# Kernel tuning notes

Hardware: AMD Instinct MI355X
Metric: run time of the kernel (lower is better)

The kernel has to match this reference:

```python
import jax, jax.numpy as jnp
import numpy as np

D_MODEL = 1024
NUM_HEADS = 16
D_HEAD = D_MODEL // NUM_HEADS
LN_EPS = 1e-5


def setup_inputs() -> dict:
    key = jax.random.key(0)
    ks = jax.random.split(key, 10)
    s = 1.0 / np.sqrt(D_MODEL)
    inp = {
        "batch": jax.random.normal(ks[0], (4, 2048, D_MODEL), dtype=jnp.float32),
        "wq": jax.random.uniform(ks[1], (D_MODEL, D_MODEL), jnp.float32, -s, s),
        "bq": jax.random.uniform(ks[2], (D_MODEL,), jnp.float32, -s, s),
        "wk": jax.random.uniform(ks[3], (D_MODEL, D_MODEL), jnp.float32, -s, s),
        "bk": jax.random.uniform(ks[4], (D_MODEL,), jnp.float32, -s, s),
        "wv": jax.random.uniform(ks[5], (D_MODEL, D_MODEL), jnp.float32, -s, s),
        "bv": jax.random.uniform(ks[6], (D_MODEL,), jnp.float32, -s, s),
        "wo": jax.random.uniform(ks[7], (D_MODEL, D_MODEL), jnp.float32, -s, s),
        "bo": jax.random.uniform(ks[8], (D_MODEL,), jnp.float32, -s, s),
        "ln_g": jnp.ones((D_MODEL,), jnp.float32),
        "ln_b": jnp.zeros((D_MODEL,), jnp.float32),
    }
    return inp


def reference(batch, wq, bq, wk, bk, wv, bv, wo, bo, ln_g, ln_b):
    B, S, D = batch.shape
    # QKV projections (torch Linear: x @ W.T + b)
    q = (batch @ wq.T + bq).reshape(B, S, NUM_HEADS, D_HEAD)
    k = (batch @ wk.T + bk).reshape(B, S, NUM_HEADS, D_HEAD)
    v = (batch @ wv.T + bv).reshape(B, S, NUM_HEADS, D_HEAD)
    # attention scores [B, H, S, S]
    scores = jnp.einsum("bqhd,bkhd->bhqk", q, k) / np.sqrt(D_HEAD).astype(np.float32)
    # (original masked_fill is not in-place -> mask has no effect; omitted)
    probs = jax.nn.softmax(scores, axis=-1)
    attn = jnp.einsum("bhqk,bkhd->bqhd", probs, v).reshape(B, S, D)
    residual = attn @ wo.T + bo  # dropout = identity (eval mode)
    x = batch + residual
    mu = jnp.mean(x, axis=-1, keepdims=True)
    var = jnp.mean(jnp.square(x - mu), axis=-1, keepdims=True)
    return (x - mu) / jnp.sqrt(var + LN_EPS) * ln_g + ln_b
```

## Files before the change

### kernel.cpp

```cpp
#include <hip/hip_runtime.h>

typedef __bf16 bf16_t;
typedef __bf16 v8bf __attribute__((ext_vector_type(8)));
typedef __bf16 v4bf __attribute__((ext_vector_type(4)));
typedef float  v4f  __attribute__((ext_vector_type(4)));

#define D_MODEL 1024
#define NHEAD   16
#define DHEAD   64
#define SEQ     2048
#define BATCH   4
#define ROWS    (BATCH*SEQ)

#define GLD16(g, l) __builtin_amdgcn_global_load_lds( \
    (const __attribute__((address_space(1))) void*)(g), \
    (__attribute__((address_space(3))) void*)(l), 16, 0, 0)

#define BAR asm volatile("s_barrier" ::: "memory")

__global__ __launch_bounds__(256) void k_prep(const float* __restrict__ batch,
                                              const float* __restrict__ wq,
                                              const float* __restrict__ wk,
                                              const float* __restrict__ wv,
                                              const float* __restrict__ wo,
                                              const float* __restrict__ bq,
                                              const float* __restrict__ bk,
                                              const float* __restrict__ bv,
                                              bf16_t* __restrict__ Xb,
                                              bf16_t* __restrict__ Wqkv,
                                              bf16_t* __restrict__ Wob,
                                              float* __restrict__ bqkv) {
    int t = threadIdx.x;
    for (int bid = blockIdx.x; bid < 12300; bid += 2048) {
        const float* src; bf16_t* dst; int idx;
        if (bid < 8192)       { src = batch; dst = Xb;             idx = bid * 256 + t; }
        else if (bid < 9216)  { src = wq;    dst = Wqkv;           idx = (bid - 8192) * 256 + t; }
        else if (bid < 10240) { src = wk;    dst = Wqkv + 1048576; idx = (bid - 9216) * 256 + t; }
        else if (bid < 11264) { src = wv;    dst = Wqkv + 2097152; idx = (bid - 10240) * 256 + t; }
        else if (bid < 12288) { src = wo;    dst = Wob;            idx = (bid - 11264) * 256 + t; }
        else {
            int i = (bid - 12288) * 256 + t;
            if (i < 1024) bqkv[i] = bq[i];
            else if (i < 2048) bqkv[i] = bk[i - 1024];
            else if (i < 3072) bqkv[i] = bv[i - 2048];
            continue;
        }
        float4 f = ((const float4*)src)[idx];
        v4bf o;
        o[0] = (bf16_t)f.x; o[1] = (bf16_t)f.y; o[2] = (bf16_t)f.z; o[3] = (bf16_t)f.w;
        ((v4bf*)dst)[idx] = o;
    }
}

__global__ __launch_bounds__(512, 2) void k_gemm256(
    const bf16_t* __restrict__ A, const bf16_t* __restrict__ Bm,
    const float* __restrict__ bias, bf16_t* __restrict__ C, float qmul)
{
    __shared__ bf16_t As[2][2][256 * 32];
    __shared__ bf16_t Bs[2][2][256 * 32];

    const int K = 1024;
    int bid = blockIdx.x;
    int wg = (bid & 7) * 48 + (bid >> 3);
    int m_idx = wg / 12, n_idx = wg % 12;
    int m0 = m_idx << 8, n0 = n_idx << 8;

    int t = threadIdx.x;
    int lane = t & 63, quad = lane >> 4, ln = lane & 15;
    int w = t >> 6, wr = w >> 2, wc = w & 3;

    int cl = (t & 3) ^ ((t >> 3) & 3);
    const bf16_t* Ag = A  + (size_t)(m0 + (t >> 2)) * K + cl * 8;
    const bf16_t* Bg = Bm + (size_t)(n0 + (t >> 2)) * K + cl * 8;
    int wb = w << 9;

#define STA(bufv, khv, kc) { const bf16_t* g_ = Ag + (kc) + ((khv) << 5); \
    GLD16(g_, &As[bufv][khv][wb]); GLD16(g_ + 131072, &As[bufv][khv][wb + 4096]); }
#define STB(bufv, khv, kc) { const bf16_t* g_ = Bg + (kc) + ((khv) << 5); \
    GLD16(g_, &Bs[bufv][khv][wb]); GLD16(g_ + 131072, &Bs[bufv][khv][wb + 4096]); }

    int rsw = (quad ^ ((ln >> 1) & 3)) << 3;
    int aofs = (wr * 128 + ln) * 32 + rsw;
    int bofs = (wc * 64 + ln) * 32 + rsw;

#define LDA(dst, bufv, mhv) { \
    dst[0] = *(const v8bf*)&AB_[aofs + (mhv) * 2048]; \
    dst[1] = *(const v8bf*)&AB_[aofs + (mhv) * 2048 + 512]; \
    dst[2] = *(const v8bf*)&AB_[aofs + (mhv) * 2048 + 1024]; \
    dst[3] = *(const v8bf*)&AB_[aofs + (mhv) * 2048 + 1536]; }
#define LDAF(dst, bufv, khv, mhv) { const bf16_t* AB_ = &As[bufv][khv][0]; LDA(dst, bufv, mhv) }
#define LDBF(dst, bufv, khv) { const bf16_t* BB_ = &Bs[bufv][khv][0]; \
    dst[0] = *(const v8bf*)&BB_[bofs]; \
    dst[1] = *(const v8bf*)&BB_[bofs + 512]; \
    dst[2] = *(const v8bf*)&BB_[bofs + 1024]; \
    dst[3] = *(const v8bf*)&BB_[bofs + 1536]; }

    v4f acc[8][4];
#pragma unroll
    for (int i = 0; i < 8; i++)
#pragma unroll
        for (int j = 0; j < 4; j++) acc[i][j] = (v4f){0.f, 0.f, 0.f, 0.f};

    v8bf aX[4], aY[4], bX[4], bY[4];

#define MF(AC, BC, M0) \
    __builtin_amdgcn_s_setprio(1); \
    acc[(M0)+0][0] = __builtin_amdgcn_mfma_f32_16x16x32_bf16(AC[0], BC[0], acc[(M0)+0][0], 0, 0, 0); \
    acc[(M0)+0][1] = __builtin_amdgcn_mfma_f32_16x16x32_bf16(AC[0], BC[1], acc[(M0)+0][1], 0, 0, 0); \
    acc[(M0)+0][2] = __builtin_amdgcn_mfma_f32_16x16x32_bf16(AC[0], BC[2], acc[(M0)+0][2], 0, 0, 0); \
    acc[(M0)+0][3] = __builtin_amdgcn_mfma_f32_16x16x32_bf16(AC[0], BC[3], acc[(M0)+0][3], 0, 0, 0); \
    acc[(M0)+1][0] = __builtin_amdgcn_mfma_f32_16x16x32_bf16(AC[1], BC[0], acc[(M0)+1][0], 0, 0, 0); \
    acc[(M0)+1][1] = __builtin_amdgcn_mfma_f32_16x16x32_bf16(AC[1], BC[1], acc[(M0)+1][1], 0, 0, 0); \
    acc[(M0)+1][2] = __builtin_amdgcn_mfma_f32_16x16x32_bf16(AC[1], BC[2], acc[(M0)+1][2], 0, 0, 0); \
    acc[(M0)+1][3] = __builtin_amdgcn_mfma_f32_16x16x32_bf16(AC[1], BC[3], acc[(M0)+1][3], 0, 0, 0); \
    acc[(M0)+2][0] = __builtin_amdgcn_mfma_f32_16x16x32_bf16(AC[2], BC[0], acc[(M0)+2][0], 0, 0, 0); \
    acc[(M0)+2][1] = __builtin_amdgcn_mfma_f32_16x16x32_bf16(AC[2], BC[1], acc[(M0)+2][1], 0, 0, 0); \
    acc[(M0)+2][2] = __builtin_amdgcn_mfma_f32_16x16x32_bf16(AC[2], BC[2], acc[(M0)+2][2], 0, 0, 0); \
    acc[(M0)+2][3] = __builtin_amdgcn_mfma_f32_16x16x32_bf16(AC[2], BC[3], acc[(M0)+2][3], 0, 0, 0); \
    acc[(M0)+3][0] = __builtin_amdgcn_mfma_f32_16x16x32_bf16(AC[3], BC[0], acc[(M0)+3][0], 0, 0, 0); \
    acc[(M0)+3][1] = __builtin_amdgcn_mfma_f32_16x16x32_bf16(AC[3], BC[1], acc[(M0)+3][1], 0, 0, 0); \
    acc[(M0)+3][2] = __builtin_amdgcn_mfma_f32_16x16x32_bf16(AC[3], BC[2], acc[(M0)+3][2], 0, 0, 0); \
    acc[(M0)+3][3] = __builtin_amdgcn_mfma_f32_16x16x32_bf16(AC[3], BC[3], acc[(M0)+3][3], 0, 0, 0); \
    __builtin_amdgcn_s_setprio(0);

#define TAIL_W6 { asm volatile("s_waitcnt vmcnt(6)" ::: "memory"); BAR; __builtin_amdgcn_sched_barrier(0); }
#define TAIL_W4 { asm volatile("s_waitcnt vmcnt(4)" ::: "memory"); BAR; __builtin_amdgcn_sched_barrier(0); }
#define TAIL_W0 { asm volatile("s_waitcnt vmcnt(0)" ::: "memory"); BAR; __builtin_amdgcn_sched_barrier(0); }

    STA(0, 0, 0); STB(0, 0, 0);
    STA(0, 1, 0); STB(0, 1, 0);
    STA(1, 0, 64); STB(1, 0, 64);
    asm volatile("s_waitcnt vmcnt(8)" ::: "memory");
    BAR; __builtin_amdgcn_sched_barrier(0);
    LDAF(aX, 0, 0, 0); LDBF(bX, 0, 0);

#define TILE(b, kc, S1, S2, S3, S4, T1, T3, P4B, P4LD) \
    S1; LDAF(aY, b, 0, 1);                    MF(aX, bX, 0); T1; \
    S2; LDBF(bY, b, 1); LDAF(aX, b, 1, 0);    MF(aY, bX, 4); \
    S3; LDAF(aY, b, 1, 1);                    MF(aX, bY, 0); T3; \
    S4; if (P4LD) { LDBF(bX, P4B, 0); LDAF(aX, P4B, 0, 0); } \
                                              MF(aY, bY, 4);

    int kb = 0;
#pragma unroll 1
    for (int tp = 0; tp < 7; ++tp, kb += 128) {
        TILE(0, kb, STA(1, 1, kb + 64), STB(1, 1, kb + 64),
                    STA(0, 0, kb + 128), STB(0, 0, kb + 128),
                    TAIL_W6, TAIL_W6, 1, 1)
        TILE(1, kb + 64, STA(0, 1, kb + 128), STB(0, 1, kb + 128),
                         STA(1, 0, kb + 192), STB(1, 0, kb + 192),
                         TAIL_W6, TAIL_W6, 0, 1)
    }
    TILE(0, 896, STA(1, 1, 960), STB(1, 1, 960), , ,
                 TAIL_W6, TAIL_W4, 1, 1)
    { const int b = 1;
      LDAF(aY, b, 0, 1);                    MF(aX, bX, 0); TAIL_W0;
      LDBF(bY, b, 1); LDAF(aX, b, 1, 0);    MF(aY, bX, 4);
      LDAF(aY, b, 1, 1);                    MF(aX, bY, 0);
                                            MF(aY, bY, 4);
    }

#undef TILE
#undef MF
#undef TAIL_W6
#undef TAIL_W4
#undef TAIL_W0
#undef LDA
#undef LDAF
#undef LDBF
#undef STA
#undef STB

#pragma unroll
    for (int m = 0; m < 8; m++) {
#pragma unroll
        for (int r = 0; r < 4; r++) {
            int row = m0 + wr * 128 + m * 16 + quad * 4 + r;
#pragma unroll
            for (int n = 0; n < 4; n++) {
                int col = n0 + wc * 64 + n * 16 + ln;
                float v = acc[m][n][r] + bias[col];
                if (col < 1024) v *= qmul;
                C[(size_t)row * 3072 + col] = (bf16_t)v;
            }
        }
    }
}

__global__ __launch_bounds__(256, 3) void k_gemm_bt(
    const bf16_t* __restrict__ A, const bf16_t* __restrict__ Bm,
    const float* __restrict__ bias, const float* __restrict__ resid,
    bf16_t* __restrict__ Cb, float* __restrict__ Cf,
    int M, int N, int K, int qcols, float qmul)
{
    __shared__ bf16_t As[2][128 * 32];
    __shared__ bf16_t Bs[2][128 * 32];

    int nTile = N >> 7;
    int x = blockIdx.x & 7, g = blockIdx.x >> 3;
    int n_idx = g % nTile;
    int m_idx = (g / nTile) * 8 + x;
    int m0 = m_idx << 7;
    int n0 = n_idx << 7;
    int t = threadIdx.x;
    int w = t >> 6, lane = t & 63, quad = lane >> 4, ln = lane & 15;
    int wm = (w >> 1) << 6, wn = (w & 1) << 6;

    int srow = lane >> 2;
    int scol = ((lane & 3) ^ ((lane >> 3) & 3)) << 3;
    const bf16_t* Ag0 = A  + (size_t)(m0 + w * 16 +      srow) * K + scol;
    const bf16_t* Ag1 = A  + (size_t)(m0 + w * 16 + 64 + srow) * K + scol;
    const bf16_t* Bg0 = Bm + (size_t)(n0 + w * 16 +      srow) * K + scol;
    const bf16_t* Bg1 = Bm + (size_t)(n0 + w * 16 + 64 + srow) * K + scol;
    int lo0 = (w * 16) * 32, lo1 = (w * 16 + 64) * 32;

    v4f acc[4][4];
#pragma unroll
    for (int i = 0; i < 4; i++)
#pragma unroll
        for (int j = 0; j < 4; j++) acc[i][j] = (v4f){0.f, 0.f, 0.f, 0.f};

    GLD16(Ag0, &As[0][lo0]);
    GLD16(Ag1, &As[0][lo1]);
    GLD16(Bg0, &Bs[0][lo0]);
    GLD16(Bg1, &Bs[0][lo1]);

    int sw = (ln >> 1) & 3;
    int buf = 0;
    for (int k0 = 0; k0 < K; k0 += 32, buf ^= 1) {
        __syncthreads();
        if (k0 + 32 < K) {
            GLD16(Ag0 + k0 + 32, &As[buf ^ 1][lo0]);
            GLD16(Ag1 + k0 + 32, &As[buf ^ 1][lo1]);
            GLD16(Bg0 + k0 + 32, &Bs[buf ^ 1][lo0]);
            GLD16(Bg1 + k0 + 32, &Bs[buf ^ 1][lo1]);
        }
        v8bf af[4], bfr[4];
#pragma unroll
        for (int mt = 0; mt < 4; mt++)
            af[mt] = *(const v8bf*)&As[buf][(wm + mt * 16 + ln) * 32 + ((quad ^ sw) << 3)];
#pragma unroll
        for (int nt = 0; nt < 4; nt++)
            bfr[nt] = *(const v8bf*)&Bs[buf][(wn + nt * 16 + ln) * 32 + ((quad ^ sw) << 3)];
#pragma unroll
        for (int mt = 0; mt < 4; mt++)
#pragma unroll
            for (int nt = 0; nt < 4; nt++)
                acc[mt][nt] = __builtin_amdgcn_mfma_f32_16x16x32_bf16(af[mt], bfr[nt], acc[mt][nt], 0, 0, 0);
    }

#pragma unroll
    for (int mt = 0; mt < 4; mt++) {
#pragma unroll
        for (int r = 0; r < 4; r++) {
            int row = m0 + wm + mt * 16 + quad * 4 + r;
#pragma unroll
            for (int nt = 0; nt < 4; nt++) {
                int col = n0 + wn + nt * 16 + ln;
                float v = acc[mt][nt][r] + bias[col];
                if (Cf) Cf[(size_t)row * N + col] = v + resid[(size_t)row * N + col];
                else {
                    if (col < qcols) v *= qmul;
                    Cb[(size_t)row * N + col] = (bf16_t)v;
                }
            }
        }
    }
}

__global__ __launch_bounds__(256) void k_transpose_v(const bf16_t* __restrict__ qkv,
                                                     bf16_t* __restrict__ vt) {
    __shared__ bf16_t tile[64 * 72];
    int bid = blockIdx.x;
    int st = bid & 31, bh = bid >> 5, b = bh >> 4, h = bh & 15;
    int t = threadIdx.x;
    const bf16_t* src = qkv + (size_t)(b * SEQ + st * 64) * 3072 + 2048 + h * 64;
#pragma unroll
    for (int i = 0; i < 2; i++) {
        int c = t + i * 256, row = c >> 3, c8 = (c & 7) << 3;
        *(uint4*)&tile[row * 72 + c8] = *(const uint4*)(src + (size_t)row * 3072 + c8);
    }
    __syncthreads();
    bf16_t* dst = vt + (size_t)bh * DHEAD * SEQ + st * 64;
#pragma unroll
    for (int i = 0; i < 2; i++) {
        int c = t + i * 256, d = c >> 3, s8 = (c & 7) << 3;
        v8bf o;
#pragma unroll
        for (int j = 0; j < 8; j++) o[j] = tile[(s8 + j) * 72 + d];
        *(v8bf*)(dst + (size_t)d * SEQ + s8) = o;
    }
}

__global__ __launch_bounds__(512, 2) void k_attn(const bf16_t* __restrict__ qkv,
                                                 const bf16_t* __restrict__ vt,
                                                 bf16_t* __restrict__ attn) {
    __shared__ bf16_t Ks[2][64 * 64];
    __shared__ bf16_t Vs[2][64 * 64];

    int bid = blockIdx.x;
    int xcd = bid & 7, u = bid >> 3;
    int qt8 = u & 7;
    int bh = ((u >> 3) << 3) | xcd;
    int b = bh >> 4, h = bh & 15;
    int t = threadIdx.x, w = t >> 6, lane = t & 63, quad = lane >> 4, ln = lane & 15;
    int q0 = qt8 * 256 + w * 32;

    v8bf qf[2][2];
#pragma unroll
    for (int qs = 0; qs < 2; qs++) {
        const bf16_t* Qp = qkv + (size_t)(b * SEQ + q0 + qs * 16 + ln) * 3072 + h * 64 + quad * 8;
        qf[qs][0] = *(const v8bf*)Qp;
        qf[qs][1] = *(const v8bf*)(Qp + 32);
    }

    int tr = w * 8 + (lane >> 3);
    int scolK = ((lane & 7) ^ ((lane >> 3) & 3) ^ ((w & 1) << 2)) << 3;
    int scolV = ((lane & 7) ^ (lane >> 3)) << 3;
    const bf16_t* Kg = qkv + (size_t)(b * SEQ + tr) * 3072 + 1024 + h * 64 + scolK;
    const bf16_t* Vg = vt + (size_t)bh * DHEAD * SEQ + (size_t)tr * SEQ + scolV;
    int ko = (w * 8) * 64;

    int gk = (ln & 3) | (((ln >> 2) & 1) << 2);
    int gv = ln & 7;
    int rrbase = ((ln >> 2) << 3) + (ln & 3);
    int o0 = (rrbase) * 64,       o1 = (rrbase + 4) * 64;
    int o2 = (rrbase + 32) * 64,  o3 = (rrbase + 36) * 64;

    const v4f z4 = (v4f){0.f, 0.f, 0.f, 0.f};
    v8bf ones8;
#pragma unroll
    for (int j = 0; j < 8; j++) ones8[j] = (bf16_t)1.0f;

    v4f o[2][4];
#pragma unroll
    for (int qs = 0; qs < 2; qs++)
#pragma unroll
        for (int d = 0; d < 4; d++) o[qs][d] = z4;
    v4f den[2] = {z4, z4};

    GLD16(Kg, &Ks[0][ko]);
    GLD16(Vg, &Vs[0][ko]);

    int buf = 0;
    for (int kt = 0; kt < SEQ; kt += 64, buf ^= 1) {
        __syncthreads();
        if (kt + 64 < SEQ) {
            GLD16(Kg + (size_t)(kt + 64) * 3072, &Ks[buf ^ 1][ko]);
            GLD16(Vg + kt + 64, &Vs[buf ^ 1][ko]);
        }

        const bf16_t* Kb = &Ks[buf][0];
        v4f s0[4], s1[4];
        int rof[4] = {o0, o1, o2, o3};
#pragma unroll
        for (int nt = 0; nt < 4; nt++) {
            v8bf kf0 = *(const v8bf*)&Kb[rof[nt] + ((quad ^ gk) << 3)];
            v8bf kf1 = *(const v8bf*)&Kb[rof[nt] + (((quad | 4) ^ gk) << 3)];
            s0[nt] = __builtin_amdgcn_mfma_f32_16x16x32_bf16(kf0, qf[0][0], z4, 0, 0, 0);
            s0[nt] = __builtin_amdgcn_mfma_f32_16x16x32_bf16(kf1, qf[0][1], s0[nt], 0, 0, 0);
            s1[nt] = __builtin_amdgcn_mfma_f32_16x16x32_bf16(kf0, qf[1][0], z4, 0, 0, 0);
            s1[nt] = __builtin_amdgcn_mfma_f32_16x16x32_bf16(kf1, qf[1][1], s1[nt], 0, 0, 0);
        }

#pragma unroll
        for (int tk = 0; tk < 2; tk++) {
            v8bf vfd[4];
#pragma unroll
            for (int d = 0; d < 4; d++)
                vfd[d] = *(const v8bf*)&Vs[buf][(d * 16 + ln) * 64 + (((tk * 4 + quad) ^ gv) << 3)];
#pragma unroll
            for (int qs = 0; qs < 2; qs++) {
                v4f* s = qs ? s1 : s0;
                float e0 = __builtin_amdgcn_exp2f(s[2 * tk][0]);
                float e1 = __builtin_amdgcn_exp2f(s[2 * tk][1]);
                float e2 = __builtin_amdgcn_exp2f(s[2 * tk][2]);
                float e3 = __builtin_amdgcn_exp2f(s[2 * tk][3]);
                float e4 = __builtin_amdgcn_exp2f(s[2 * tk + 1][0]);
                float e5 = __builtin_amdgcn_exp2f(s[2 * tk + 1][1]);
                float e6 = __builtin_amdgcn_exp2f(s[2 * tk + 1][2]);
                float e7 = __builtin_amdgcn_exp2f(s[2 * tk + 1][3]);
                v8bf pf;
                pf[0] = (bf16_t)e0; pf[1] = (bf16_t)e1; pf[2] = (bf16_t)e2; pf[3] = (bf16_t)e3;
                pf[4] = (bf16_t)e4; pf[5] = (bf16_t)e5; pf[6] = (bf16_t)e6; pf[7] = (bf16_t)e7;
                den[qs] = __builtin_amdgcn_mfma_f32_16x16x32_bf16(pf, ones8, den[qs], 0, 0, 0);
#pragma unroll
                for (int d = 0; d < 4; d++)
                    o[qs][d] = __builtin_amdgcn_mfma_f32_16x16x32_bf16(pf, vfd[d], o[qs][d], 0, 0, 0);
            }
        }
    }

#pragma unroll
    for (int qs = 0; qs < 2; qs++) {
        int rowg = b * SEQ + q0 + qs * 16;
#pragma unroll
        for (int r = 0; r < 4; r++) {
            float inv = 1.f / den[qs][r];
#pragma unroll
            for (int d = 0; d < 4; d++)
                attn[(size_t)(rowg + quad * 4 + r) * D_MODEL + h * 64 + d * 16 + ln] =
                    (bf16_t)(o[qs][d][r] * inv);
        }
    }
}

__global__ __launch_bounds__(256) void k_layernorm(const float* __restrict__ y,
                                                   const float* __restrict__ g,
                                                   const float* __restrict__ beta,
                                                   float* __restrict__ out) {
    __shared__ float rs[4], rq[4];
    int row = blockIdx.x, t = threadIdx.x;
    int w = t >> 6, lane = t & 63;
    float4 v = ((const float4*)(y + (size_t)row * D_MODEL))[t];
    float s = v.x + v.y + v.z + v.w;
    float q = v.x * v.x + v.y * v.y + v.z * v.z + v.w * v.w;
#pragma unroll
    for (int off = 1; off < 64; off <<= 1) {
        s += __shfl_xor(s, off);
        q += __shfl_xor(q, off);
    }
    if (lane == 0) { rs[w] = s; rq[w] = q; }
    __syncthreads();
    s = rs[0] + rs[1] + rs[2] + rs[3];
    q = rq[0] + rq[1] + rq[2] + rq[3];
    float mu = s * (1.f / D_MODEL);
    float var = q * (1.f / D_MODEL) - mu * mu;
    float rstd = rsqrtf(var + 1e-5f);
    float4 gg = ((const float4*)g)[t];
    float4 bb = ((const float4*)beta)[t];
    float4 o;
    o.x = (v.x - mu) * rstd * gg.x + bb.x;
    o.y = (v.y - mu) * rstd * gg.y + bb.y;
    o.z = (v.z - mu) * rstd * gg.z + bb.z;
    o.w = (v.w - mu) * rstd * gg.w + bb.w;
    ((float4*)(out + (size_t)row * D_MODEL))[t] = o;
}

extern "C" void kernel_launch(void* const* d_in, const int* in_sizes, int n_in,
                              void* d_out, int out_size, void* d_ws, size_t ws_size,
                              hipStream_t stream) {
    const float* batch = (const float*)d_in[0];
    const float* wq = (const float*)d_in[1];
    const float* bq = (const float*)d_in[2];
    const float* wk = (const float*)d_in[3];
    const float* bk = (const float*)d_in[4];
    const float* wv = (const float*)d_in[5];
    const float* bv = (const float*)d_in[6];
    const float* wo = (const float*)d_in[7];
    const float* bo = (const float*)d_in[8];
    const float* ln_g = (const float*)d_in[9];
    const float* ln_b = (const float*)d_in[10];
    float* out = (float*)d_out;

    char* ws = (char*)d_ws;
    size_t offXb   = 0;
    size_t offWqkv = offXb + (size_t)ROWS * D_MODEL * 2;
    size_t offWo   = offWqkv + (size_t)3072 * 1024 * 2;
    size_t offBias = offWo + (size_t)1024 * 1024 * 2;
    size_t offQKV  = offBias + 3072 * 4;
    size_t offAttn = offQKV + (size_t)ROWS * 3072 * 2;
    size_t total   = offAttn + (size_t)ROWS * D_MODEL * 2;
    if (ws_size < total) return;

    bf16_t* Xb   = (bf16_t*)(ws + offXb);
    bf16_t* Vt   = (bf16_t*)(ws + offXb);
    bf16_t* Wqkv = (bf16_t*)(ws + offWqkv);
    bf16_t* Wob  = (bf16_t*)(ws + offWo);
    float*  bqkv = (float*)(ws + offBias);
    bf16_t* qkv  = (bf16_t*)(ws + offQKV);
    float*  y    = (float*)(ws + offQKV);
    bf16_t* attn = (bf16_t*)(ws + offAttn);

    const float SC = 0.125f * 1.44269504088896f;

    k_prep<<<2048, 256, 0, stream>>>(batch, wq, wk, wv, wo, bq, bk, bv,
                                     Xb, Wqkv, Wob, bqkv);
    k_gemm256<<<384, 512, 0, stream>>>(Xb, Wqkv, bqkv, qkv, SC);
    k_transpose_v<<<2048, 256, 0, stream>>>(qkv, Vt);
    k_attn<<<512, 512, 0, stream>>>(qkv, Vt, attn);
    k_gemm_bt<<<64 * 8, 256, 0, stream>>>(attn, Wob, bo, batch, nullptr, y,
                                          8192, 1024, 1024, 0, 1.0f);
    k_layernorm<<<8192, 256, 0, stream>>>(y, ln_g, ln_b, out);
}
```

Measured before the change: 289.1 us.

## Fuse V projection with transpose into dedicated GEMM epilogue, drop transpose kernel

The QKV GEMM now computes only Q and K into a narrower 2048-column buffer. A new 128x128 GEMM kernel computes V, adds the bias, transposes the tile through swizzled shared memory and writes V^T directly in the per-head layout that attention reads. This removes the separate transpose kernel and the round trip of V through global memory. In exchange, V runs on a smaller-tile GEMM that may be less efficient than the 256-tile kernel, and the workspace no longer aliases Vt with Xb.

```diff
diff --git a/kernel.cpp b/kernel.cpp
--- a/kernel.cpp
+++ b/kernel.cpp
@@ -61,8 +61,8 @@
 
     const int K = 1024;
     int bid = blockIdx.x;
-    int wg = (bid & 7) * 48 + (bid >> 3);
-    int m_idx = wg / 12, n_idx = wg % 12;
+    int wg = (bid & 7) * 32 + (bid >> 3);
+    int m_idx = wg >> 3, n_idx = wg & 7;
     int m0 = m_idx << 8, n0 = n_idx << 8;
 
     int t = threadIdx.x;
@@ -181,20 +181,18 @@
                 int col = n0 + wc * 64 + n * 16 + ln;
                 float v = acc[m][n][r] + bias[col];
                 if (col < 1024) v *= qmul;
-                C[(size_t)row * 3072 + col] = (bf16_t)v;
+                C[(size_t)row * 2048 + col] = (bf16_t)v;
             }
         }
     }
 }
 
-__global__ __launch_bounds__(256, 3) void k_gemm_bt(
+__global__ __launch_bounds__(256, 3) void k_gemm_vt(
     const bf16_t* __restrict__ A, const bf16_t* __restrict__ Bm,
-    const float* __restrict__ bias, const float* __restrict__ resid,
-    bf16_t* __restrict__ Cb, float* __restrict__ Cf,
-    int M, int N, int K, int qcols, float qmul)
+    const float* __restrict__ bias, bf16_t* __restrict__ vt)
 {
-    __shared__ bf16_t As[2][128 * 32];
-    __shared__ bf16_t Bs[2][128 * 32];
+    __shared__ bf16_t SH[4][128 * 32];
+    const int K = 1024, N = 1024;
 
     int nTile = N >> 7;
     int x = blockIdx.x & 7, g = blockIdx.x >> 3;
@@ -220,6 +218,103 @@
 #pragma unroll
         for (int j = 0; j < 4; j++) acc[i][j] = (v4f){0.f, 0.f, 0.f, 0.f};
 
+    GLD16(Ag0, &SH[0][lo0]);
+    GLD16(Ag1, &SH[0][lo1]);
+    GLD16(Bg0, &SH[2][lo0]);
+    GLD16(Bg1, &SH[2][lo1]);
+
+    int sw = (ln >> 1) & 3;
+    int buf = 0;
+    for (int k0 = 0; k0 < K; k0 += 32, buf ^= 1) {
+        __syncthreads();
+        if (k0 + 32 < K) {
+            GLD16(Ag0 + k0 + 32, &SH[buf ^ 1][lo0]);
+            GLD16(Ag1 + k0 + 32, &SH[buf ^ 1][lo1]);
+            GLD16(Bg0 + k0 + 32, &SH[2 + (buf ^ 1)][lo0]);
+            GLD16(Bg1 + k0 + 32, &SH[2 + (buf ^ 1)][lo1]);
+        }
+        v8bf af[4], bfr[4];
+#pragma unroll
+        for (int mt = 0; mt < 4; mt++)
+            af[mt] = *(const v8bf*)&SH[buf][(wm + mt * 16 + ln) * 32 + ((quad ^ sw) << 3)];
+#pragma unroll
+        for (int nt = 0; nt < 4; nt++)
+            bfr[nt] = *(const v8bf*)&SH[2 + buf][(wn + nt * 16 + ln) * 32 + ((quad ^ sw) << 3)];
+#pragma unroll
+        for (int mt = 0; mt < 4; mt++)
+#pragma unroll
+            for (int nt = 0; nt < 4; nt++)
+                acc[mt][nt] = __builtin_amdgcn_mfma_f32_16x16x32_bf16(af[mt], bfr[nt], acc[mt][nt], 0, 0, 0);
+    }
+
+    __syncthreads();
+    bf16_t* P = &SH[0][0];
+#pragma unroll
+    for (int mt = 0; mt < 4; mt++) {
+#pragma unroll
+        for (int r = 0; r < 4; r++) {
+            int s_loc = wm + mt * 16 + quad * 4 + r;
+            int swz = ((s_loc >> 3) & 15) << 1;
+#pragma unroll
+            for (int nt = 0; nt < 4; nt++) {
+                int d_loc = wn + nt * 16 + ln;
+                float v = acc[mt][nt][r] + bias[n0 + d_loc];
+                P[s_loc * 128 + (d_loc ^ swz)] = (bf16_t)v;
+            }
+        }
+    }
+    __syncthreads();
+    int b = m0 >> 11, sBase = m0 & 2047;
+#pragma unroll
+    for (int i = 0; i < 8; i++) {
+        int gidx = t + i * 256;
+        int d = gidx >> 4;
+        int s0 = (gidx & 15) << 3;
+        v8bf o;
+#pragma unroll
+        for (int j = 0; j < 8; j++) {
+            int s = s0 + j;
+            o[j] = P[s * 128 + (d ^ (((s >> 3) & 15) << 1))];
+        }
+        int col = n0 + d;
+        int h = col >> 6, dh = col & 63;
+        *(v8bf*)(vt + (size_t)(b * 16 + h) * DHEAD * SEQ + (size_t)dh * SEQ + sBase + s0) = o;
+    }
+}
+
+__global__ __launch_bounds__(256, 3) void k_gemm_bt(
+    const bf16_t* __restrict__ A, const bf16_t* __restrict__ Bm,
+    const float* __restrict__ bias, const float* __restrict__ resid,
+    bf16_t* __restrict__ Cb, float* __restrict__ Cf,
+    int M, int N, int K, int qcols, float qmul)
+{
+    __shared__ bf16_t As[2][128 * 32];
+    __shared__ bf16_t Bs[2][128 * 32];
+
+    int nTile = N >> 7;
+    int x = blockIdx.x & 7, g = blockIdx.x >> 3;
+    int n_idx = g % nTile;
+    int m_idx = (g / nTile) * 8 + x;
+    int m0 = m_idx << 7;
+    int n0 = n_idx << 7;
+    int t = threadIdx.x;
+    int w = t >> 6, lane = t & 63, quad = lane >> 4, ln = lane & 15;
+    int wm = (w >> 1) << 6, wn = (w & 1) << 6;
+
+    int srow = lane >> 2;
+    int scol = ((lane & 3) ^ ((lane >> 3) & 3)) << 3;
+    const bf16_t* Ag0 = A  + (size_t)(m0 + w * 16 +      srow) * K + scol;
+    const bf16_t* Ag1 = A  + (size_t)(m0 + w * 16 + 64 + srow) * K + scol;
+    const bf16_t* Bg0 = Bm + (size_t)(n0 + w * 16 +      srow) * K + scol;
+    const bf16_t* Bg1 = Bm + (size_t)(n0 + w * 16 + 64 + srow) * K + scol;
+    int lo0 = (w * 16) * 32, lo1 = (w * 16 + 64) * 32;
+
+    v4f acc[4][4];
+#pragma unroll
+    for (int i = 0; i < 4; i++)
+#pragma unroll
+        for (int j = 0; j < 4; j++) acc[i][j] = (v4f){0.f, 0.f, 0.f, 0.f};
+
     GLD16(Ag0, &As[0][lo0]);
     GLD16(Ag1, &As[0][lo1]);
     GLD16(Bg0, &Bs[0][lo0]);
@@ -268,31 +363,7 @@
     }
 }
 
-__global__ __launch_bounds__(256) void k_transpose_v(const bf16_t* __restrict__ qkv,
-                                                     bf16_t* __restrict__ vt) {
-    __shared__ bf16_t tile[64 * 72];
-    int bid = blockIdx.x;
-    int st = bid & 31, bh = bid >> 5, b = bh >> 4, h = bh & 15;
-    int t = threadIdx.x;
-    const bf16_t* src = qkv + (size_t)(b * SEQ + st * 64) * 3072 + 2048 + h * 64;
-#pragma unroll
-    for (int i = 0; i < 2; i++) {
-        int c = t + i * 256, row = c >> 3, c8 = (c & 7) << 3;
-        *(uint4*)&tile[row * 72 + c8] = *(const uint4*)(src + (size_t)row * 3072 + c8);
-    }
-    __syncthreads();
-    bf16_t* dst = vt + (size_t)bh * DHEAD * SEQ + st * 64;
-#pragma unroll
-    for (int i = 0; i < 2; i++) {
-        int c = t + i * 256, d = c >> 3, s8 = (c & 7) << 3;
-        v8bf o;
-#pragma unroll
-        for (int j = 0; j < 8; j++) o[j] = tile[(s8 + j) * 72 + d];
-        *(v8bf*)(dst + (size_t)d * SEQ + s8) = o;
-    }
-}
-
-__global__ __launch_bounds__(512, 2) void k_attn(const bf16_t* __restrict__ qkv,
+__global__ __launch_bounds__(512, 2) void k_attn(const bf16_t* __restrict__ qk,
                                                  const bf16_t* __restrict__ vt,
                                                  bf16_t* __restrict__ attn) {
     __shared__ bf16_t Ks[2][64 * 64];
@@ -309,7 +380,7 @@
     v8bf qf[2][2];
 #pragma unroll
     for (int qs = 0; qs < 2; qs++) {
-        const bf16_t* Qp = qkv + (size_t)(b * SEQ + q0 + qs * 16 + ln) * 3072 + h * 64 + quad * 8;
+        const bf16_t* Qp = qk + (size_t)(b * SEQ + q0 + qs * 16 + ln) * 2048 + h * 64 + quad * 8;
         qf[qs][0] = *(const v8bf*)Qp;
         qf[qs][1] = *(const v8bf*)(Qp + 32);
     }
@@ -317,7 +388,7 @@
     int tr = w * 8 + (lane >> 3);
     int scolK = ((lane & 7) ^ ((lane >> 3) & 3) ^ ((w & 1) << 2)) << 3;
     int scolV = ((lane & 7) ^ (lane >> 3)) << 3;
-    const bf16_t* Kg = qkv + (size_t)(b * SEQ + tr) * 3072 + 1024 + h * 64 + scolK;
+    const bf16_t* Kg = qk + (size_t)(b * SEQ + tr) * 2048 + 1024 + h * 64 + scolK;
     const bf16_t* Vg = vt + (size_t)bh * DHEAD * SEQ + (size_t)tr * SEQ + scolV;
     int ko = (w * 8) * 64;
 
@@ -346,7 +417,7 @@
     for (int kt = 0; kt < SEQ; kt += 64, buf ^= 1) {
         __syncthreads();
         if (kt + 64 < SEQ) {
-            GLD16(Kg + (size_t)(kt + 64) * 3072, &Ks[buf ^ 1][ko]);
+            GLD16(Kg + (size_t)(kt + 64) * 2048, &Ks[buf ^ 1][ko]);
             GLD16(Vg + kt + 64, &Vs[buf ^ 1][ko]);
         }
 
@@ -458,27 +529,28 @@
     size_t offWqkv = offXb + (size_t)ROWS * D_MODEL * 2;
     size_t offWo   = offWqkv + (size_t)3072 * 1024 * 2;
     size_t offBias = offWo + (size_t)1024 * 1024 * 2;
-    size_t offQKV  = offBias + 3072 * 4;
-    size_t offAttn = offQKV + (size_t)ROWS * 3072 * 2;
+    size_t offQK   = offBias + 3072 * 4;
+    size_t offVt   = offQK + (size_t)ROWS * 2048 * 2;
+    size_t offAttn = offVt + (size_t)64 * DHEAD * SEQ * 2;
     size_t total   = offAttn + (size_t)ROWS * D_MODEL * 2;
     if (ws_size < total) return;
 
     bf16_t* Xb   = (bf16_t*)(ws + offXb);
-    bf16_t* Vt   = (bf16_t*)(ws + offXb);
     bf16_t* Wqkv = (bf16_t*)(ws + offWqkv);
     bf16_t* Wob  = (bf16_t*)(ws + offWo);
     float*  bqkv = (float*)(ws + offBias);
-    bf16_t* qkv  = (bf16_t*)(ws + offQKV);
-    float*  y    = (float*)(ws + offQKV);
+    bf16_t* qk   = (bf16_t*)(ws + offQK);
+    float*  y    = (float*)(ws + offQK);
+    bf16_t* Vt   = (bf16_t*)(ws + offVt);
     bf16_t* attn = (bf16_t*)(ws + offAttn);
 
     const float SC = 0.125f * 1.44269504088896f;
 
     k_prep<<<2048, 256, 0, stream>>>(batch, wq, wk, wv, wo, bq, bk, bv,
                                      Xb, Wqkv, Wob, bqkv);
-    k_gemm256<<<384, 512, 0, stream>>>(Xb, Wqkv, bqkv, qkv, SC);
-    k_transpose_v<<<2048, 256, 0, stream>>>(qkv, Vt);
-    k_attn<<<512, 512, 0, stream>>>(qkv, Vt, attn);
+    k_gemm256<<<256, 512, 0, stream>>>(Xb, Wqkv, bqkv, qk, SC);
+    k_gemm_vt<<<64 * 8, 256, 0, stream>>>(Xb, Wqkv + 2097152, bqkv + 2048, Vt);
+    k_attn<<<512, 512, 0, stream>>>(qk, Vt, attn);
     k_gemm_bt<<<64 * 8, 256, 0, stream>>>(attn, Wob, bo, batch, nullptr, y,
                                           8192, 1024, 1024, 0, 1.0f);
     k_layernorm<<<8192, 256, 0, stream>>>(y, ln_g, ln_b, out);
```

Measured after the change: 278.7 us. 3.6% less time.
